# Performance work log

Hardware: AMD Instinct MI355X
Metric: run time of the kernel (lower is better)

The kernel has to match this reference:

```python
import jax, jax.numpy as jnp
import numpy as np

HID = 2048      # hidden_size
NH = 32         # num_heads
G = 8           # num_kv_groups
R = NH // G     # repeat factor (heads per kv group)
HD = HID // NH  # head_dim = 64
SCALE = HD ** 0.5


def setup_inputs() -> dict:
    key = jax.random.key(0)
    ks = jax.random.split(key, 10)
    B, S = 2, 1024
    x = jax.random.normal(ks[0], (B, S, HID), dtype=jnp.float32)
    attention_mask = jnp.ones((B, S, S), dtype=jnp.float32)
    # Linear params stored as [in, out] (y = x @ W + b), same math as torch Linear.
    Wq = jax.random.normal(ks[1], (HID, HID), dtype=jnp.float32) * 0.02
    bq = jnp.zeros((HID,), dtype=jnp.float32)
    Wk = jax.random.normal(ks[2], (HID, G * HD), dtype=jnp.float32) * 0.02
    bk = jnp.zeros((G * HD,), dtype=jnp.float32)
    Wv = jax.random.normal(ks[3], (HID, G * HD), dtype=jnp.float32) * 0.02
    bv = jnp.zeros((G * HD,), dtype=jnp.float32)
    Wo = jax.random.normal(ks[4], (HID, HID), dtype=jnp.float32) * 0.02
    bo = jnp.zeros((HID,), dtype=jnp.float32)
    return {"x": x, "attention_mask": attention_mask,
            "Wq": Wq, "bq": bq, "Wk": Wk, "bk": bk,
            "Wv": Wv, "bv": bv, "Wo": Wo, "bo": bo}


def reference(x, attention_mask, Wq, bq, Wk, bk, Wv, bv, Wo, bo):
    B, S, _ = x.shape
    # Projections. Group heads as (G, R) instead of repeat_interleave:
    # repeat_interleave(key, R, dim=2) duplicates each kv group R times, which is
    # exactly sharing key[:, :, g] across the R heads of group g.
    q = (x @ Wq + bq).reshape(B, S, G, R, HD)   # [B,S,G,R,HD] (heads = G*R in order)
    k = (x @ Wk + bk).reshape(B, S, G, HD)      # [B,S,G,HD]
    v = (x @ Wv + bv).reshape(B, S, G, HD)
    # scores [B,G,R,Sq,Sk] == torch's [B, NH, Sq, Sk] with NH = G*R
    scores = jnp.einsum('bqgrd,bkgd->bgrqk', q, k) / SCALE
    scores = scores * attention_mask[:, None, None]  # multiplicative mask per head
    w = jax.nn.softmax(scores, axis=-1)
    out = jnp.einsum('bgrqk,bkgd->bqgrd', w, v).reshape(B, S, HID)
    return out @ Wo + bo + x
```

## Files before the change

### kernel.cpp

```cpp
#include <hip/hip_runtime.h>

typedef unsigned short u16;
typedef unsigned int u32;
typedef __attribute__((ext_vector_type(8))) short bf16x8;
typedef __attribute__((ext_vector_type(4))) float f32x4;

#define HID 2048
#define S_LEN 1024
#define BATCH 2
#define G_KV 8
#define R_REP 4
#define HD 64
#define NQKV 3072

__device__ __forceinline__ u16 f2bf(float f) {
    union { u32 u; float ff; } x; x.ff = f;
    u32 u = x.u;
    u += 0x7FFFu + ((u >> 16) & 1u);
    return (u16)(u >> 16);
}

__device__ __forceinline__ void gload_lds16(const void* g, void* l) {
    __builtin_amdgcn_global_load_lds((const __attribute__((address_space(1))) void*)g,
                                     (__attribute__((address_space(3))) void*)l,
                                     16, 0, 0);
}

__global__ __launch_bounds__(256) void prep(const float* __restrict__ x,
                                            const float* __restrict__ Wq,
                                            const float* __restrict__ Wk,
                                            const float* __restrict__ Wv,
                                            const float* __restrict__ Wo,
                                            u16* __restrict__ Xb,
                                            u16* __restrict__ WqkvT,
                                            u16* __restrict__ WoT) {
    __shared__ float tile[64][65];
    int bid = blockIdx.x, tid = threadIdx.x;

    if (bid < 2048) {
        int i = (bid * 256 + tid) * 8;
        float4 a = *(const float4*)(x + i);
        float4 b = *(const float4*)(x + i + 4);
        u16 t[8] = {f2bf(a.x), f2bf(a.y), f2bf(a.z), f2bf(a.w),
                    f2bf(b.x), f2bf(b.y), f2bf(b.z), f2bf(b.w)};
        *(uint4*)(Xb + i) = *(const uint4*)t;
        return;
    }

    int w = tid >> 6, lane = tid & 63;
    const float* in; int N, n0, k0, nc0; u16* outp;
    if (bid < 3584) {
        int local = bid - 2048;
        n0 = (local % 48) * 64; k0 = (local / 48) * 64;
        if (n0 < 2048)      { in = Wq; N = 2048; nc0 = n0; }
        else if (n0 < 2560) { in = Wk; N = 512;  nc0 = n0 - 2048; }
        else                { in = Wv; N = 512;  nc0 = n0 - 2560; }
        outp = WqkvT;
    } else {
        int local = bid - 3584;
        n0 = (local & 31) * 64; k0 = (local >> 5) * 64;
        in = Wo; N = 2048; nc0 = n0; outp = WoT;
    }

#pragma unroll
    for (int p = 0; p < 16; ++p)
        tile[w * 16 + p][lane] = in[(size_t)(k0 + w * 16 + p) * N + nc0 + lane];
    __syncthreads();

    int nrow = lane >> 4, kk = (lane & 15) * 4;
#pragma unroll
    for (int j = 0; j < 16; j += 4) {
        int n = w * 16 + j + nrow;
        u32 w0 = (u32)f2bf(tile[kk][n])     | ((u32)f2bf(tile[kk + 1][n]) << 16);
        u32 w1 = (u32)f2bf(tile[kk + 2][n]) | ((u32)f2bf(tile[kk + 3][n]) << 16);
        uint2 pk; pk.x = w0; pk.y = w1;
        *(uint2*)&outp[(size_t)(n0 + n) * 2048 + k0 + kk] = pk;
    }
}

__global__ __launch_bounds__(256) void gemm_qkv(const u16* __restrict__ Xb,
                                                const u16* __restrict__ WT,
                                                const float* __restrict__ bq,
                                                const float* __restrict__ bk,
                                                const float* __restrict__ bv,
                                                u16* __restrict__ qb,
                                                u16* __restrict__ kb,
                                                u16* __restrict__ vb) {
    __shared__ __align__(16) u16 As[2][64 * 32];
    __shared__ __align__(16) u16 Bs[2][128 * 32];
    int tid = threadIdx.x;
    int w = tid >> 6, lane = tid & 63, quad = lane >> 4, l16 = lane & 15;
    int m0 = blockIdx.y * 64, n0 = blockIdx.x * 128;
    int wr = (w >> 1) * 32, wc = (w & 1) * 64;
    int srow = lane >> 2, scol = (lane & 3) * 8;

    const u16* aP  = &Xb[(size_t)(m0 + w * 16 + srow) * 2048 + scol];
    const u16* bP0 = &WT[(size_t)(n0 + w * 32 + srow) * 2048 + scol];
    const u16* bP1 = &WT[(size_t)(n0 + w * 32 + 16 + srow) * 2048 + scol];

    f32x4 acc[2][4];
#pragma unroll
    for (int i = 0; i < 2; ++i)
#pragma unroll
        for (int j = 0; j < 4; ++j) acc[i][j] = (f32x4){0.f, 0.f, 0.f, 0.f};

    gload_lds16(aP,  &As[0][(w * 16) * 32]);
    gload_lds16(bP0, &Bs[0][(w * 32) * 32]);
    gload_lds16(bP1, &Bs[0][(w * 32 + 16) * 32]);
    __syncthreads();

    int cur = 0;
    for (int k0 = 0; k0 < 2048; k0 += 32) {
        int kn = k0 + 32;
        if (kn < 2048) {
            gload_lds16(aP + kn,  &As[cur ^ 1][(w * 16) * 32]);
            gload_lds16(bP0 + kn, &Bs[cur ^ 1][(w * 32) * 32]);
            gload_lds16(bP1 + kn, &Bs[cur ^ 1][(w * 32 + 16) * 32]);
        }
        bf16x8 af[2], bfr[4];
#pragma unroll
        for (int mt = 0; mt < 2; ++mt)
            af[mt] = *(const bf16x8*)&As[cur][(wr + mt * 16 + l16) * 32 + quad * 8];
#pragma unroll
        for (int nt = 0; nt < 4; ++nt)
            bfr[nt] = *(const bf16x8*)&Bs[cur][(wc + nt * 16 + l16) * 32 + quad * 8];
#pragma unroll
        for (int mt = 0; mt < 2; ++mt)
#pragma unroll
            for (int nt = 0; nt < 4; ++nt)
                acc[mt][nt] = __builtin_amdgcn_mfma_f32_16x16x32_bf16(af[mt], bfr[nt], acc[mt][nt], 0, 0, 0);
        __syncthreads();
        cur ^= 1;
    }

#pragma unroll
    for (int nt = 0; nt < 4; ++nt) {
        int n = n0 + wc + nt * 16 + l16;
        float bias;
        if (n < 2048) bias = bq[n];
        else if (n < 2560) bias = bk[n - 2048];
        else bias = bv[n - 2560];
#pragma unroll
        for (int mt = 0; mt < 2; ++mt) {
#pragma unroll
            for (int reg = 0; reg < 4; ++reg) {
                int m = m0 + wr + mt * 16 + quad * 4 + reg;
                float val = acc[mt][nt][reg] + bias;
                int b = m >> 10, s = m & 1023;
                if (n < 2048) {
                    int g = n >> 8, r = (n >> 6) & 3, d = n & 63;
                    qb[((((size_t)(b * G_KV + g) * R_REP + r) * S_LEN) + s) * HD + d] = f2bf(val * 0.125f);
                } else if (n < 2560) {
                    int n2 = n - 2048, g = n2 >> 6, d = n2 & 63;
                    kb[(((size_t)(b * G_KV + g) * S_LEN) + s) * HD + d] = f2bf(val);
                } else {
                    int n2 = n - 2560, g = n2 >> 6, d = n2 & 63;
                    vb[(((size_t)(b * G_KV + g) * HD + d) * S_LEN) + s] = f2bf(val);
                }
            }
        }
    }
}

__global__ __launch_bounds__(256) void attn_mfma(const u16* __restrict__ qbuf,
                                                 const u16* __restrict__ kbuf,
                                                 const u16* __restrict__ vtbuf,
                                                 const float* __restrict__ mask,
                                                 u16* __restrict__ aout) {
    __shared__ __align__(16) u16 Ks[64 * 72];
    __shared__ __align__(16) u16 Vs[64 * 72];
    __shared__ __align__(16) u16 Ps[2][64 * 72];
    __shared__ __align__(16) float Ms[32 * 68];
    __shared__ float l_lds[128];

    int d = blockIdx.x;
    int qblk = d & 31, g = (d >> 5) & 7, b = d >> 8;
    int s0 = qblk * 32;

    int tid = threadIdx.x;
    int w = tid >> 6, lane = tid & 63, quad = lane >> 4, l16 = lane & 15;
    int qs = w * 16 + l16;

    const u16* qrow = qbuf +
        ((((size_t)(b * G_KV + g) * R_REP + w) * S_LEN) + s0 + l16) * HD;
    bf16x8 qf0_lo = *(const bf16x8*)(qrow + quad * 8);
    bf16x8 qf1_lo = *(const bf16x8*)(qrow + 32 + quad * 8);
    bf16x8 qf0_hi = *(const bf16x8*)(qrow + 16 * HD + quad * 8);
    bf16x8 qf1_hi = *(const bf16x8*)(qrow + 16 * HD + 32 + quad * 8);

    f32x4 o_lo[4], o_hi[4];
#pragma unroll
    for (int i = 0; i < 4; ++i) {
        o_lo[i] = (f32x4){0.f, 0.f, 0.f, 0.f};
        o_hi[i] = (f32x4){0.f, 0.f, 0.f, 0.f};
    }
    float l_lo = 0.f, l_hi = 0.f;

    const u16* kbase  = kbuf  + (size_t)(b * G_KV + g) * S_LEN * HD;
    const u16* vtbase = vtbuf + (size_t)(b * G_KV + g) * HD * S_LEN;
    int msrow = tid >> 3, mscol = (tid & 7) * 8;
    const float* mstage = mask + ((size_t)b * S_LEN + s0 + msrow) * S_LEN + mscol;

    int srow = tid >> 2, sc = (tid & 3) * 16;

    uint4 kp0, kp1, vp0, vp1;
    f32x4 mp0, mp1;
    {
        const u16* kr = kbase + (size_t)srow * HD + sc;
        kp0 = *(const uint4*)kr; kp1 = *(const uint4*)(kr + 8);
        const u16* vr = vtbase + (size_t)srow * S_LEN + sc;
        vp0 = *(const uint4*)vr; vp1 = *(const uint4*)(vr + 8);
        mp0 = *(const f32x4*)mstage; mp1 = *(const f32x4*)(mstage + 4);
    }

    for (int kt = 0; kt < 16; ++kt) {
        __syncthreads();
        *(uint4*)&Ks[srow * 72 + sc]     = kp0;
        *(uint4*)&Ks[srow * 72 + sc + 8] = kp1;
        *(uint4*)&Vs[srow * 72 + sc]     = vp0;
        *(uint4*)&Vs[srow * 72 + sc + 8] = vp1;
        *(f32x4*)&Ms[msrow * 68 + mscol]     = mp0;
        *(f32x4*)&Ms[msrow * 68 + mscol + 4] = mp1;
        __syncthreads();

        if (kt < 15) {
            int nk = (kt + 1) * 64;
            const u16* kr = kbase + (size_t)(nk + srow) * HD + sc;
            kp0 = *(const uint4*)kr; kp1 = *(const uint4*)(kr + 8);
            const u16* vr = vtbase + (size_t)srow * S_LEN + nk + sc;
            vp0 = *(const uint4*)vr; vp1 = *(const uint4*)(vr + 8);
            mp0 = *(const f32x4*)(mstage + nk);
            mp1 = *(const f32x4*)(mstage + nk + 4);
        }

#pragma unroll
        for (int mt = 0; mt < 4; ++mt) {
            bf16x8 af0 = *(const bf16x8*)&Ks[(mt * 16 + l16) * 72 + quad * 8];
            bf16x8 af1 = *(const bf16x8*)&Ks[(mt * 16 + l16) * 72 + 32 + quad * 8];
            f32x4 z0 = (f32x4){0.f, 0.f, 0.f, 0.f};
            z0 = __builtin_amdgcn_mfma_f32_16x16x32_bf16(af0, qf0_lo, z0, 0, 0, 0);
            f32x4 s_lo = __builtin_amdgcn_mfma_f32_16x16x32_bf16(af1, qf1_lo, z0, 0, 0, 0);
            f32x4 z1 = (f32x4){0.f, 0.f, 0.f, 0.f};
            z1 = __builtin_amdgcn_mfma_f32_16x16x32_bf16(af0, qf0_hi, z1, 0, 0, 0);
            f32x4 s_hi = __builtin_amdgcn_mfma_f32_16x16x32_bf16(af1, qf1_hi, z1, 0, 0, 0);

            f32x4 mv_lo = *(const f32x4*)&Ms[l16 * 68 + mt * 16 + quad * 4];
            f32x4 mv_hi = *(const f32x4*)&Ms[(16 + l16) * 68 + mt * 16 + quad * 4];

            u32 er[4];
#pragma unroll
            for (int rg = 0; rg < 4; ++rg) {
                float e = __expf(s_lo[rg] * mv_lo[rg]);
                u32 u = __float_as_uint(e) + 0x8000u;
                er[rg] = u;
                l_lo += __uint_as_float(u & 0xFFFF0000u);
            }
            uint2 pk;
            pk.x = __builtin_amdgcn_perm(er[1], er[0], 0x07060302u);
            pk.y = __builtin_amdgcn_perm(er[3], er[2], 0x07060302u);
            *(uint2*)&Ps[0][qs * 72 + mt * 16 + quad * 4] = pk;

#pragma unroll
            for (int rg = 0; rg < 4; ++rg) {
                float e = __expf(s_hi[rg] * mv_hi[rg]);
                u32 u = __float_as_uint(e) + 0x8000u;
                er[rg] = u;
                l_hi += __uint_as_float(u & 0xFFFF0000u);
            }
            pk.x = __builtin_amdgcn_perm(er[1], er[0], 0x07060302u);
            pk.y = __builtin_amdgcn_perm(er[3], er[2], 0x07060302u);
            *(uint2*)&Ps[1][qs * 72 + mt * 16 + quad * 4] = pk;
        }

        bf16x8 pf0_lo = *(const bf16x8*)&Ps[0][qs * 72 + quad * 8];
        bf16x8 pf1_lo = *(const bf16x8*)&Ps[0][qs * 72 + 32 + quad * 8];
        bf16x8 pf0_hi = *(const bf16x8*)&Ps[1][qs * 72 + quad * 8];
        bf16x8 pf1_hi = *(const bf16x8*)&Ps[1][qs * 72 + 32 + quad * 8];
#pragma unroll
        for (int nt = 0; nt < 4; ++nt) {
            bf16x8 vf0 = *(const bf16x8*)&Vs[(nt * 16 + l16) * 72 + quad * 8];
            bf16x8 vf1 = *(const bf16x8*)&Vs[(nt * 16 + l16) * 72 + 32 + quad * 8];
            o_lo[nt] = __builtin_amdgcn_mfma_f32_16x16x32_bf16(pf0_lo, vf0, o_lo[nt], 0, 0, 0);
            o_lo[nt] = __builtin_amdgcn_mfma_f32_16x16x32_bf16(pf1_lo, vf1, o_lo[nt], 0, 0, 0);
            o_hi[nt] = __builtin_amdgcn_mfma_f32_16x16x32_bf16(pf0_hi, vf0, o_hi[nt], 0, 0, 0);
            o_hi[nt] = __builtin_amdgcn_mfma_f32_16x16x32_bf16(pf1_hi, vf1, o_hi[nt], 0, 0, 0);
        }
    }

    l_lo += __shfl_xor(l_lo, 16);
    l_lo += __shfl_xor(l_lo, 32);
    l_hi += __shfl_xor(l_hi, 16);
    l_hi += __shfl_xor(l_hi, 32);
    l_lds[qs] = l_lo;
    l_lds[64 + qs] = l_hi;

#pragma unroll
    for (int reg = 0; reg < 4; ++reg) {
        int qloc = quad * 4 + reg;
        float inv_lo = 1.0f / l_lds[w * 16 + qloc];
        float inv_hi = 1.0f / l_lds[64 + w * 16 + qloc];
        u16* dst_lo = aout + ((size_t)(b * S_LEN + s0 + qloc)) * HID + (g * R_REP + w) * HD;
        u16* dst_hi = dst_lo + (size_t)16 * HID;
#pragma unroll
        for (int nt = 0; nt < 4; ++nt) {
            dst_lo[nt * 16 + l16] = f2bf(o_lo[nt][reg] * inv_lo);
            dst_hi[nt * 16 + l16] = f2bf(o_hi[nt][reg] * inv_hi);
        }
    }
}

__global__ __launch_bounds__(256) void gemm_o(const u16* __restrict__ A,
                                              const u16* __restrict__ WT,
                                              const float* __restrict__ bo,
                                              const float* __restrict__ Xres,
                                              float* __restrict__ out) {
    __shared__ __align__(16) u16 As[2][64 * 32];
    __shared__ __align__(16) u16 Bs[2][128 * 32];
    int tid = threadIdx.x;
    int w = tid >> 6, lane = tid & 63, quad = lane >> 4, l16 = lane & 15;
    int m0 = blockIdx.y * 64, n0 = blockIdx.x * 128;
    int wr = (w >> 1) * 32, wc = (w & 1) * 64;
    int srow = lane >> 2, scol = (lane & 3) * 8;

    const u16* aP  = &A[(size_t)(m0 + w * 16 + srow) * 2048 + scol];
    const u16* bP0 = &WT[(size_t)(n0 + w * 32 + srow) * 2048 + scol];
    const u16* bP1 = &WT[(size_t)(n0 + w * 32 + 16 + srow) * 2048 + scol];

    f32x4 acc[2][4];
#pragma unroll
    for (int i = 0; i < 2; ++i)
#pragma unroll
        for (int j = 0; j < 4; ++j) acc[i][j] = (f32x4){0.f, 0.f, 0.f, 0.f};

    gload_lds16(aP,  &As[0][(w * 16) * 32]);
    gload_lds16(bP0, &Bs[0][(w * 32) * 32]);
    gload_lds16(bP1, &Bs[0][(w * 32 + 16) * 32]);
    __syncthreads();

    int cur = 0;
    for (int k0 = 0; k0 < 2048; k0 += 32) {
        int kn = k0 + 32;
        if (kn < 2048) {
            gload_lds16(aP + kn,  &As[cur ^ 1][(w * 16) * 32]);
            gload_lds16(bP0 + kn, &Bs[cur ^ 1][(w * 32) * 32]);
            gload_lds16(bP1 + kn, &Bs[cur ^ 1][(w * 32 + 16) * 32]);
        }
        bf16x8 af[2], bfr[4];
#pragma unroll
        for (int mt = 0; mt < 2; ++mt)
            af[mt] = *(const bf16x8*)&As[cur][(wr + mt * 16 + l16) * 32 + quad * 8];
#pragma unroll
        for (int nt = 0; nt < 4; ++nt)
            bfr[nt] = *(const bf16x8*)&Bs[cur][(wc + nt * 16 + l16) * 32 + quad * 8];
#pragma unroll
        for (int mt = 0; mt < 2; ++mt)
#pragma unroll
            for (int nt = 0; nt < 4; ++nt)
                acc[mt][nt] = __builtin_amdgcn_mfma_f32_16x16x32_bf16(af[mt], bfr[nt], acc[mt][nt], 0, 0, 0);
        __syncthreads();
        cur ^= 1;
    }

#pragma unroll
    for (int nt = 0; nt < 4; ++nt) {
        int n = n0 + wc + nt * 16 + l16;
        float bias = bo[n];
#pragma unroll
        for (int mt = 0; mt < 2; ++mt) {
#pragma unroll
            for (int reg = 0; reg < 4; ++reg) {
                int m = m0 + wr + mt * 16 + quad * 4 + reg;
                out[(size_t)m * 2048 + n] = acc[mt][nt][reg] + bias + Xres[(size_t)m * 2048 + n];
            }
        }
    }
}

extern "C" void kernel_launch(void* const* d_in, const int* in_sizes, int n_in,
                              void* d_out, int out_size, void* d_ws, size_t ws_size,
                              hipStream_t stream) {
    const float* x    = (const float*)d_in[0];
    const float* mask = (const float*)d_in[1];
    const float* Wq   = (const float*)d_in[2];
    const float* bq   = (const float*)d_in[3];
    const float* Wk   = (const float*)d_in[4];
    const float* bk   = (const float*)d_in[5];
    const float* Wv   = (const float*)d_in[6];
    const float* bv   = (const float*)d_in[7];
    const float* Wo   = (const float*)d_in[8];
    const float* bo   = (const float*)d_in[9];
    float* out = (float*)d_out;

    u16* ws = (u16*)d_ws;
    size_t off = 0;
    u16* WqkvT = ws + off; off += (size_t)NQKV * 2048;
    u16* WoT   = ws + off; off += (size_t)2048 * 2048;
    u16* q_buf = ws + off; off += (size_t)BATCH * G_KV * R_REP * S_LEN * HD;
    u16* k_buf = ws + off; off += (size_t)BATCH * G_KV * S_LEN * HD;
    u16* v_buf = ws + off; off += (size_t)BATCH * G_KV * S_LEN * HD;
    u16* a_out = ws + off; off += (size_t)2048 * 2048;
    u16* Xb    = a_out;

    prep<<<dim3(4608), 256, 0, stream>>>(x, Wq, Wk, Wv, Wo, Xb, WqkvT, WoT);

    gemm_qkv<<<dim3(NQKV / 128, 2048 / 64), 256, 0, stream>>>(Xb, WqkvT, bq, bk, bv,
                                                              q_buf, k_buf, v_buf);

    attn_mfma<<<dim3(BATCH * G_KV * 32), 256, 0, stream>>>(
        q_buf, k_buf, v_buf, mask, a_out);

    gemm_o<<<dim3(2048 / 128, 2048 / 64), 256, 0, stream>>>(a_out, WoT, bo, x, out);
}
```

Baseline: 235.9 us.

## Split K across two wave groups in QKV and output GEMMs

Both projection GEMMs now launch 512 threads per block, with two independent groups of four waves each computing half of the K=2048 reduction using their own double-buffered LDS region. The second group writes its partial accumulators to shared memory, and the first group adds them before applying bias and the epilogue. The aim is more waves per block, hiding memory latency and halving the serial K-loop length, at the cost of more LDS (48KB per block), an extra reduction pass through LDS, and possibly lower block occupancy.

```diff
diff --git a/kernel.cpp b/kernel.cpp
--- a/kernel.cpp
+++ b/kernel.cpp
@@ -78,7 +78,7 @@
     }
 }
 
-__global__ __launch_bounds__(256) void gemm_qkv(const u16* __restrict__ Xb,
+__global__ __launch_bounds__(512) void gemm_qkv(const u16* __restrict__ Xb,
                                                 const u16* __restrict__ WT,
                                                 const float* __restrict__ bq,
                                                 const float* __restrict__ bk,
@@ -86,17 +86,22 @@
                                                 u16* __restrict__ qb,
                                                 u16* __restrict__ kb,
                                                 u16* __restrict__ vb) {
-    __shared__ __align__(16) u16 As[2][64 * 32];
-    __shared__ __align__(16) u16 Bs[2][128 * 32];
+    __shared__ __align__(16) char smem[49152];
     int tid = threadIdx.x;
     int w = tid >> 6, lane = tid & 63, quad = lane >> 4, l16 = lane & 15;
+    int half = w >> 2, ws = w & 3;
     int m0 = blockIdx.y * 64, n0 = blockIdx.x * 128;
-    int wr = (w >> 1) * 32, wc = (w & 1) * 64;
+    int wr = (ws >> 1) * 32, wc = (ws & 1) * 64;
     int srow = lane >> 2, scol = (lane & 3) * 8;
 
-    const u16* aP  = &Xb[(size_t)(m0 + w * 16 + srow) * 2048 + scol];
-    const u16* bP0 = &WT[(size_t)(n0 + w * 32 + srow) * 2048 + scol];
-    const u16* bP1 = &WT[(size_t)(n0 + w * 32 + 16 + srow) * 2048 + scol];
+    u16* A0 = (u16*)(smem + half * 24576);
+    u16* A1 = (u16*)(smem + half * 24576 + 4096);
+    u16* B0 = (u16*)(smem + half * 24576 + 8192);
+    u16* B1 = (u16*)(smem + half * 24576 + 16384);
+
+    const u16* aP  = &Xb[(size_t)(m0 + ws * 16 + srow) * 2048 + half * 1024 + scol];
+    const u16* bP0 = &WT[(size_t)(n0 + ws * 32 + srow) * 2048 + half * 1024 + scol];
+    const u16* bP1 = bP0 + (size_t)16 * 2048;
 
     f32x4 acc[2][4];
 #pragma unroll
@@ -104,26 +109,28 @@
 #pragma unroll
         for (int j = 0; j < 4; ++j) acc[i][j] = (f32x4){0.f, 0.f, 0.f, 0.f};
 
-    gload_lds16(aP,  &As[0][(w * 16) * 32]);
-    gload_lds16(bP0, &Bs[0][(w * 32) * 32]);
-    gload_lds16(bP1, &Bs[0][(w * 32 + 16) * 32]);
+    gload_lds16(aP,  A0 + (ws * 16) * 32);
+    gload_lds16(bP0, B0 + (ws * 32) * 32);
+    gload_lds16(bP1, B0 + (ws * 32 + 16) * 32);
     __syncthreads();
 
     int cur = 0;
-    for (int k0 = 0; k0 < 2048; k0 += 32) {
+    for (int k0 = 0; k0 < 1024; k0 += 32) {
         int kn = k0 + 32;
-        if (kn < 2048) {
-            gload_lds16(aP + kn,  &As[cur ^ 1][(w * 16) * 32]);
-            gload_lds16(bP0 + kn, &Bs[cur ^ 1][(w * 32) * 32]);
-            gload_lds16(bP1 + kn, &Bs[cur ^ 1][(w * 32 + 16) * 32]);
+        u16* Ac = cur ? A1 : A0; u16* Bc = cur ? B1 : B0;
+        u16* An = cur ? A0 : A1; u16* Bn = cur ? B0 : B1;
+        if (kn < 1024) {
+            gload_lds16(aP + kn,  An + (ws * 16) * 32);
+            gload_lds16(bP0 + kn, Bn + (ws * 32) * 32);
+            gload_lds16(bP1 + kn, Bn + (ws * 32 + 16) * 32);
         }
         bf16x8 af[2], bfr[4];
 #pragma unroll
         for (int mt = 0; mt < 2; ++mt)
-            af[mt] = *(const bf16x8*)&As[cur][(wr + mt * 16 + l16) * 32 + quad * 8];
+            af[mt] = *(const bf16x8*)&Ac[(wr + mt * 16 + l16) * 32 + quad * 8];
 #pragma unroll
         for (int nt = 0; nt < 4; ++nt)
-            bfr[nt] = *(const bf16x8*)&Bs[cur][(wc + nt * 16 + l16) * 32 + quad * 8];
+            bfr[nt] = *(const bf16x8*)&Bc[(wc + nt * 16 + l16) * 32 + quad * 8];
 #pragma unroll
         for (int mt = 0; mt < 2; ++mt)
 #pragma unroll
@@ -133,29 +140,43 @@
         cur ^= 1;
     }
 
-#pragma unroll
-    for (int nt = 0; nt < 4; ++nt) {
-        int n = n0 + wc + nt * 16 + l16;
-        float bias;
-        if (n < 2048) bias = bq[n];
-        else if (n < 2560) bias = bk[n - 2048];
-        else bias = bv[n - 2560];
-#pragma unroll
-        for (int mt = 0; mt < 2; ++mt) {
-#pragma unroll
-            for (int reg = 0; reg < 4; ++reg) {
-                int m = m0 + wr + mt * 16 + quad * 4 + reg;
-                float val = acc[mt][nt][reg] + bias;
-                int b = m >> 10, s = m & 1023;
-                if (n < 2048) {
-                    int g = n >> 8, r = (n >> 6) & 3, d = n & 63;
-                    qb[((((size_t)(b * G_KV + g) * R_REP + r) * S_LEN) + s) * HD + d] = f2bf(val * 0.125f);
-                } else if (n < 2560) {
-                    int n2 = n - 2048, g = n2 >> 6, d = n2 & 63;
-                    kb[(((size_t)(b * G_KV + g) * S_LEN) + s) * HD + d] = f2bf(val);
-                } else {
-                    int n2 = n - 2560, g = n2 >> 6, d = n2 & 63;
-                    vb[(((size_t)(b * G_KV + g) * HD + d) * S_LEN) + s] = f2bf(val);
+    float* red = (float*)smem;
+    if (half == 1) {
+        int t0 = tid - 256;
+#pragma unroll
+        for (int mt = 0; mt < 2; ++mt)
+#pragma unroll
+            for (int nt = 0; nt < 4; ++nt)
+#pragma unroll
+                for (int reg = 0; reg < 4; ++reg)
+                    red[t0 * 33 + (mt * 4 + nt) * 4 + reg] = acc[mt][nt][reg];
+    }
+    __syncthreads();
+    if (half == 0) {
+#pragma unroll
+        for (int nt = 0; nt < 4; ++nt) {
+            int n = n0 + wc + nt * 16 + l16;
+            float bias;
+            if (n < 2048) bias = bq[n];
+            else if (n < 2560) bias = bk[n - 2048];
+            else bias = bv[n - 2560];
+#pragma unroll
+            for (int mt = 0; mt < 2; ++mt) {
+#pragma unroll
+                for (int reg = 0; reg < 4; ++reg) {
+                    int m = m0 + wr + mt * 16 + quad * 4 + reg;
+                    float val = acc[mt][nt][reg] + red[tid * 33 + (mt * 4 + nt) * 4 + reg] + bias;
+                    int b = m >> 10, s = m & 1023;
+                    if (n < 2048) {
+                        int g = n >> 8, r = (n >> 6) & 3, d = n & 63;
+                        qb[((((size_t)(b * G_KV + g) * R_REP + r) * S_LEN) + s) * HD + d] = f2bf(val * 0.125f);
+                    } else if (n < 2560) {
+                        int n2 = n - 2048, g = n2 >> 6, d = n2 & 63;
+                        kb[(((size_t)(b * G_KV + g) * S_LEN) + s) * HD + d] = f2bf(val);
+                    } else {
+                        int n2 = n - 2560, g = n2 >> 6, d = n2 & 63;
+                        vb[(((size_t)(b * G_KV + g) * HD + d) * S_LEN) + s] = f2bf(val);
+                    }
                 }
             }
         }
@@ -309,22 +330,27 @@
     }
 }
 
-__global__ __launch_bounds__(256) void gemm_o(const u16* __restrict__ A,
+__global__ __launch_bounds__(512) void gemm_o(const u16* __restrict__ A,
                                               const u16* __restrict__ WT,
                                               const float* __restrict__ bo,
                                               const float* __restrict__ Xres,
                                               float* __restrict__ out) {
-    __shared__ __align__(16) u16 As[2][64 * 32];
-    __shared__ __align__(16) u16 Bs[2][128 * 32];
+    __shared__ __align__(16) char smem[49152];
     int tid = threadIdx.x;
     int w = tid >> 6, lane = tid & 63, quad = lane >> 4, l16 = lane & 15;
+    int half = w >> 2, ws = w & 3;
     int m0 = blockIdx.y * 64, n0 = blockIdx.x * 128;
-    int wr = (w >> 1) * 32, wc = (w & 1) * 64;
+    int wr = (ws >> 1) * 32, wc = (ws & 1) * 64;
     int srow = lane >> 2, scol = (lane & 3) * 8;
 
-    const u16* aP  = &A[(size_t)(m0 + w * 16 + srow) * 2048 + scol];
-    const u16* bP0 = &WT[(size_t)(n0 + w * 32 + srow) * 2048 + scol];
-    const u16* bP1 = &WT[(size_t)(n0 + w * 32 + 16 + srow) * 2048 + scol];
+    u16* A0 = (u16*)(smem + half * 24576);
+    u16* A1 = (u16*)(smem + half * 24576 + 4096);
+    u16* B0 = (u16*)(smem + half * 24576 + 8192);
+    u16* B1 = (u16*)(smem + half * 24576 + 16384);
+
+    const u16* aP  = &A[(size_t)(m0 + ws * 16 + srow) * 2048 + half * 1024 + scol];
+    const u16* bP0 = &WT[(size_t)(n0 + ws * 32 + srow) * 2048 + half * 1024 + scol];
+    const u16* bP1 = bP0 + (size_t)16 * 2048;
 
     f32x4 acc[2][4];
 #pragma unroll
@@ -332,26 +358,28 @@
 #pragma unroll
         for (int j = 0; j < 4; ++j) acc[i][j] = (f32x4){0.f, 0.f, 0.f, 0.f};
 
-    gload_lds16(aP,  &As[0][(w * 16) * 32]);
-    gload_lds16(bP0, &Bs[0][(w * 32) * 32]);
-    gload_lds16(bP1, &Bs[0][(w * 32 + 16) * 32]);
+    gload_lds16(aP,  A0 + (ws * 16) * 32);
+    gload_lds16(bP0, B0 + (ws * 32) * 32);
+    gload_lds16(bP1, B0 + (ws * 32 + 16) * 32);
     __syncthreads();
 
     int cur = 0;
-    for (int k0 = 0; k0 < 2048; k0 += 32) {
+    for (int k0 = 0; k0 < 1024; k0 += 32) {
         int kn = k0 + 32;
-        if (kn < 2048) {
-            gload_lds16(aP + kn,  &As[cur ^ 1][(w * 16) * 32]);
-            gload_lds16(bP0 + kn, &Bs[cur ^ 1][(w * 32) * 32]);
-            gload_lds16(bP1 + kn, &Bs[cur ^ 1][(w * 32 + 16) * 32]);
+        u16* Ac = cur ? A1 : A0; u16* Bc = cur ? B1 : B0;
+        u16* An = cur ? A0 : A1; u16* Bn = cur ? B0 : B1;
+        if (kn < 1024) {
+            gload_lds16(aP + kn,  An + (ws * 16) * 32);
+            gload_lds16(bP0 + kn, Bn + (ws * 32) * 32);
+            gload_lds16(bP1 + kn, Bn + (ws * 32 + 16) * 32);
         }
         bf16x8 af[2], bfr[4];
 #pragma unroll
         for (int mt = 0; mt < 2; ++mt)
-            af[mt] = *(const bf16x8*)&As[cur][(wr + mt * 16 + l16) * 32 + quad * 8];
+            af[mt] = *(const bf16x8*)&Ac[(wr + mt * 16 + l16) * 32 + quad * 8];
 #pragma unroll
         for (int nt = 0; nt < 4; ++nt)
-            bfr[nt] = *(const bf16x8*)&Bs[cur][(wc + nt * 16 + l16) * 32 + quad * 8];
+            bfr[nt] = *(const bf16x8*)&Bc[(wc + nt * 16 + l16) * 32 + quad * 8];
 #pragma unroll
         for (int mt = 0; mt < 2; ++mt)
 #pragma unroll
@@ -361,16 +389,31 @@
         cur ^= 1;
     }
 
-#pragma unroll
-    for (int nt = 0; nt < 4; ++nt) {
-        int n = n0 + wc + nt * 16 + l16;
-        float bias = bo[n];
-#pragma unroll
-        for (int mt = 0; mt < 2; ++mt) {
-#pragma unroll
-            for (int reg = 0; reg < 4; ++reg) {
-                int m = m0 + wr + mt * 16 + quad * 4 + reg;
-                out[(size_t)m * 2048 + n] = acc[mt][nt][reg] + bias + Xres[(size_t)m * 2048 + n];
+    float* red = (float*)smem;
+    if (half == 1) {
+        int t0 = tid - 256;
+#pragma unroll
+        for (int mt = 0; mt < 2; ++mt)
+#pragma unroll
+            for (int nt = 0; nt < 4; ++nt)
+#pragma unroll
+                for (int reg = 0; reg < 4; ++reg)
+                    red[t0 * 33 + (mt * 4 + nt) * 4 + reg] = acc[mt][nt][reg];
+    }
+    __syncthreads();
+    if (half == 0) {
+#pragma unroll
+        for (int nt = 0; nt < 4; ++nt) {
+            int n = n0 + wc + nt * 16 + l16;
+            float bias = bo[n];
+#pragma unroll
+            for (int mt = 0; mt < 2; ++mt) {
+#pragma unroll
+                for (int reg = 0; reg < 4; ++reg) {
+                    int m = m0 + wr + mt * 16 + quad * 4 + reg;
+                    float val = acc[mt][nt][reg] + red[tid * 33 + (mt * 4 + nt) * 4 + reg];
+                    out[(size_t)m * 2048 + n] = val + bias + Xres[(size_t)m * 2048 + n];
+                }
             }
         }
     }
@@ -403,11 +446,11 @@
 
     prep<<<dim3(4608), 256, 0, stream>>>(x, Wq, Wk, Wv, Wo, Xb, WqkvT, WoT);
 
-    gemm_qkv<<<dim3(NQKV / 128, 2048 / 64), 256, 0, stream>>>(Xb, WqkvT, bq, bk, bv,
+    gemm_qkv<<<dim3(NQKV / 128, 2048 / 64), 512, 0, stream>>>(Xb, WqkvT, bq, bk, bv,
                                                               q_buf, k_buf, v_buf);
 
     attn_mfma<<<dim3(BATCH * G_KV * 32), 256, 0, stream>>>(
         q_buf, k_buf, v_buf, mask, a_out);
 
-    gemm_o<<<dim3(2048 / 128, 2048 / 64), 256, 0, stream>>>(a_out, WoT, bo, x, out);
-}
+    gemm_o<<<dim3(2048 / 128, 2048 / 64), 512, 0, stream>>>(a_out, WoT, bo, x, out);
+}
```

After: 234.2 us. No clear change (-0.7%).
